# Kernel optimization log

Hardware: AMD Instinct MI355X
Metric: run time of the kernel (lower is better)

## Reference

```python
import jax, jax.numpy as jnp
import numpy as np

N = 65536      # nodes
E = 1048576    # edges (avg degree 16)
B = 64         # graphs in batch
H = 128        # hidden
L = 3          # message-passing layers
MAXZ = 100


def _segment_mean(x, idx, n):
    s = jax.ops.segment_sum(x, idx, num_segments=n)
    c = jax.ops.segment_sum(jnp.ones((idx.shape[0], 1), x.dtype), idx, num_segments=n)
    return s / jnp.maximum(c, 1.0)


def setup_inputs() -> dict:
    key = jax.random.key(0)
    ks = jax.random.split(key, 24)
    w = lambda k, shape: jax.random.normal(k, shape, dtype=jnp.float32) * 0.05
    inp = {
        "pos": jax.random.normal(ks[0], (N, 3), dtype=jnp.float32),
        "z": jax.random.randint(ks[1], (N,), 0, MAXZ),
        "batch": jnp.sort(jax.random.randint(ks[2], (N,), 0, B)),
        "edge_index": jax.random.randint(ks[3], (2, E), 0, N),
        "node_type": jax.random.randint(ks[4], (N,), 0, 2),
        # parameters (weights stored [in, out] so y = x @ W + b)
        "emb": w(ks[5], (MAXZ, H)),
        "lin_in_w": w(ks[6], (H + 3, H)),
        "lin_in_b": jnp.zeros((H,), jnp.float32),
        "msg_w1": w(ks[7], (L, 2 * H + 1, H)),
        "msg_b1": jnp.zeros((L, H), jnp.float32),
        "msg_w2": w(ks[8], (L, H, H)),
        "msg_b2": jnp.zeros((L, H), jnp.float32),
        "upd_w": w(ks[9], (L, 2 * H, H)),
        "upd_b": jnp.zeros((L, H), jnp.float32),
        "ro_w1": w(ks[10], (H, H)),
        "ro_b1": jnp.zeros((H,), jnp.float32),
        "ro_w2": w(ks[11], (H, 1)),
        "ro_b2": jnp.zeros((1,), jnp.float32),
    }
    return inp


def reference(pos, z, batch, edge_index, node_type,
              emb, lin_in_w, lin_in_b,
              msg_w1, msg_b1, msg_w2, msg_b2,
              upd_w, upd_b, ro_w1, ro_b1, ro_w2, ro_b2):
    # centroid-centered positions per graph
    center = _segment_mean(pos, batch, B)           # [B,3]
    pos_rel = pos - center[batch]                   # [N,3]

    x = jnp.concatenate([emb[z], pos_rel], axis=-1) @ lin_in_w + lin_in_b  # [N,H]

    row, col = edge_index[0], edge_index[1]
    rel = pos_rel[col] - pos_rel[row]               # [E,3]
    dist = jnp.linalg.norm(rel, axis=-1, keepdims=True)  # [E,1]

    for l in range(L):
        m_in = jnp.concatenate([x[col], x[row], dist], axis=-1)      # [E,2H+1]
        h = jax.nn.relu(m_in @ msg_w1[l] + msg_b1[l])
        m_ij = jax.nn.relu(h @ msg_w2[l] + msg_b2[l])                # [E,H] (dropout=identity, eval)
        m_i = _segment_mean(m_ij, row, N)                            # [N,H]
        x = jax.nn.relu(jnp.concatenate([x, m_i], axis=-1) @ upd_w[l] + upd_b[l])

    lig_mask = (node_type == 1).astype(x.dtype)                      # [N]
    lig_counts = jnp.maximum(jax.ops.segment_sum(lig_mask, batch, num_segments=B), 1.0)
    g = jax.ops.segment_sum(x * lig_mask[:, None], batch, num_segments=B)  # [B,H]
    g = g / lig_counts[:, None]

    hg = jax.nn.relu(g @ ro_w1 + ro_b1)
    affinity = (hg @ ro_w2 + ro_b2).squeeze(-1)                      # [B]
    return affinity
```

## Files before the change

kernel.cpp:

```cpp
#include <hip/hip_runtime.h>
#include <hip/hip_bf16.h>
#include <hip/hip_fp16.h>
#include <math.h>

#define NN 65536
#define NE 1048576
#define NB 64
#define HD 128
#define NL 3

#define O_CSUM   0
#define O_CCNT   192
#define O_LCNT   256
#define O_GSUM   320
#define O_DEGI   8512
#define O_POSREL 74048
#define O_RC     270656
#define O_XHI    1319232
#define O_XLO    5513536
#define O_P      9707840
#define O_RCD    13902144
#define O_Q      18096448
#define O_C1H    22290752
#define O_EW     22291456
#define O_MSUM   26485056
#define O_W2T    34873664
#define O_W1TH   34898240
#define O_W1TL   34947392
#define O_WUTH   34996544
#define O_WUTL   35045696
#define O_CHK    35094848

typedef __attribute__((ext_vector_type(8))) short bf16x8;
typedef __attribute__((ext_vector_type(8))) _Float16 f16x8;
typedef __attribute__((ext_vector_type(8))) unsigned short u16x8;
typedef __attribute__((ext_vector_type(4))) float f32x4;

__device__ __forceinline__ void atomAdd(float* p, float v) { unsafeAtomicAdd(p, v); }

__device__ __forceinline__ unsigned short f2bf(float f) {
    union { __hip_bfloat16 h; unsigned short u; } cv;
    cv.h = __float2bfloat16(f);
    return cv.u;
}
__device__ __forceinline__ float bf2f(unsigned short u) {
    union { float f; unsigned v; } c; c.v = ((unsigned)u) << 16; return c.f;
}
__device__ __forceinline__ void split2(float v, unsigned short& h, unsigned short& l) {
    h = f2bf(v); l = f2bf(v - bf2f(h));
}
__device__ __forceinline__ unsigned short f2h(float f) {
    union { __half h; unsigned short u; } c; c.h = __float2half(f); return c.u;
}

__global__ __launch_bounds__(256) void stats_kernel(
    const float* __restrict__ pos, const int* __restrict__ batch,
    const int* __restrict__ ntype,
    float* __restrict__ csum, float* __restrict__ ccnt, float* __restrict__ lcnt)
{
    __shared__ float s[NB * 5];
    const int tid = threadIdx.x;
    for (int i = tid; i < NB * 5; i += 256) s[i] = 0.f;
    __syncthreads();
    const int n = blockIdx.x * 256 + tid;
    const int b = batch[n];
    atomicAdd(&s[b*5+0], pos[n*3+0]);
    atomicAdd(&s[b*5+1], pos[n*3+1]);
    atomicAdd(&s[b*5+2], pos[n*3+2]);
    atomicAdd(&s[b*5+3], 1.f);
    if (ntype[n] == 1) atomicAdd(&s[b*5+4], 1.f);
    __syncthreads();
    for (int i = tid; i < NB * 5; i += 256) {
        float v = s[i];
        if (v != 0.f) {
            int b2 = i / 5, f = i - b2*5;
            if (f < 3)       atomAdd(&csum[b2*3+f], v);
            else if (f == 3) atomAdd(&ccnt[b2], v);
            else             atomAdd(&lcnt[b2], v);
        }
    }
}

__global__ __launch_bounds__(256) void deg_kernel(const int* __restrict__ row, int* __restrict__ degi)
{
    const int e = blockIdx.x * 256 + threadIdx.x;
    atomicAdd(&degi[row[e]], 1);
}

__global__ __launch_bounds__(256) void scanA_kernel(const int* __restrict__ degi, int* __restrict__ chunkSum)
{
    __shared__ int red[4];
    const int t = threadIdx.x, b = blockIdx.x;
    int v = degi[b*256 + t];
    #pragma unroll
    for (int off = 32; off > 0; off >>= 1) v += __shfl_down(v, off, 64);
    if ((t & 63) == 0) red[t >> 6] = v;
    __syncthreads();
    if (t == 0) chunkSum[b] = red[0] + red[1] + red[2] + red[3];
}

__global__ __launch_bounds__(256) void scanB_kernel(int* __restrict__ chunkSum)
{
    __shared__ int s[256];
    const int t = threadIdx.x;
    const int v = chunkSum[t];
    s[t] = v;
    __syncthreads();
    #pragma unroll
    for (int off = 1; off < 256; off <<= 1) {
        int u = (t >= off) ? s[t - off] : 0;
        __syncthreads();
        s[t] += u;
        __syncthreads();
    }
    chunkSum[t] = s[t] - v;
}

__global__ __launch_bounds__(256) void scanC_kernel(const int* __restrict__ degi,
                                                    const int* __restrict__ chunkOff,
                                                    int* __restrict__ rowStart)
{
    __shared__ int s[256];
    const int t = threadIdx.x, b = blockIdx.x;
    const int v = degi[b*256 + t];
    s[t] = v;
    __syncthreads();
    #pragma unroll
    for (int off = 1; off < 256; off <<= 1) {
        int u = (t >= off) ? s[t - off] : 0;
        __syncthreads();
        s[t] += u;
        __syncthreads();
    }
    rowStart[b*256 + t] = chunkOff[b] + s[t] - v;
}

__global__ __launch_bounds__(256) void scatter_kernel(
    const int* __restrict__ row, const int* __restrict__ col,
    const int* __restrict__ rowStart, int* __restrict__ cnt,
    uint2* __restrict__ rcD,
    const float* __restrict__ posrel)
{
    const int e = blockIdx.x * 256 + threadIdx.x;
    const int r = row[e], c = col[e];
    const float dx = posrel[c*3+0] - posrel[r*3+0];
    const float dy = posrel[c*3+1] - posrel[r*3+1];
    const float dz = posrel[c*3+2] - posrel[r*3+2];
    const float dist = sqrtf(dx*dx + dy*dy + dz*dz);
    const int p = rowStart[r] + atomicAdd(&cnt[r], 1);
    rcD[p] = make_uint2(((unsigned)r << 16) | (unsigned)c, __float_as_uint(dist));
}

__global__ __launch_bounds__(256) void posrel_kernel(
    const float* __restrict__ pos, const int* __restrict__ batch,
    const float* __restrict__ csum, const float* __restrict__ ccnt,
    float* __restrict__ posrel)
{
    const int n = blockIdx.x * 256 + threadIdx.x;
    const int b = batch[n];
    const float inv = 1.f / fmaxf(ccnt[b], 1.f);
    posrel[n*3+0] = pos[n*3+0] - csum[b*3+0]*inv;
    posrel[n*3+1] = pos[n*3+1] - csum[b*3+1]*inv;
    posrel[n*3+2] = pos[n*3+2] - csum[b*3+2]*inv;
}

__global__ __launch_bounds__(256) void wprep_kernel(
    const float* __restrict__ mw1, const float* __restrict__ uw,
    const float* __restrict__ mw2,
    const float* __restrict__ lin_w, const float* __restrict__ lin_b,
    const float* __restrict__ emb,
    unsigned short* __restrict__ w1th, unsigned short* __restrict__ w1tl,
    unsigned short* __restrict__ wuth, unsigned short* __restrict__ wutl,
    unsigned short* __restrict__ w2t, unsigned short* __restrict__ c1h,
    float* __restrict__ EW)
{
    const int idx = blockIdx.x * 256 + threadIdx.x;
    {
        const int l = idx >> 15, rem = idx & 32767;
        const int w = rem & 7, t = rem >> 3;
        const int c = t & 255, kb = t >> 8;
        const int k = kb*8 + w;
        const int kk = (c < 128) ? k : (128 + k);
        const int cc = c & 127;
        const float v = mw1[l*257*128 + kk*128 + cc];
        unsigned short h, lo; split2(v, h, lo);
        w1th[idx] = h; w1tl[idx] = lo;
    }
    {
        const int l = idx >> 15, rem = idx & 32767;
        const int w = rem & 7, t = rem >> 3;
        const int c = t & 127, kb = t >> 7;
        const int k = kb*8 + w;
        const float v = uw[l*256*128 + k*128 + c];
        unsigned short h, lo; split2(v, h, lo);
        wuth[idx] = h; wutl[idx] = lo;
    }
    if (idx < 49152) {
        const int l = idx >> 14, rem = idx & 16383;
        const int blk = rem >> 3, win = rem & 7;
        const int n = blk >> 4, cs = blk & 15;
        const int c = cs ^ (n & 7);
        const int k = c*8 + win;
        w2t[idx] = f2h(mw2[(l << 14) + k*128 + n]);
    }
    if (idx < 384) {
        const int l = idx >> 7, c = idx & 127;
        c1h[idx] = f2h(mw1[l*257*128 + 256*128 + c]);
    }
    if (idx < 12800) {
        const int j = idx & 127, zz = idx >> 7;
        float acc = lin_b[j];
        for (int k = 0; k < 128; ++k)
            acc += emb[zz*128 + k] * lin_w[k*128 + j];
        EW[idx] = acc;
    }
}

__global__ __launch_bounds__(256) void lin_in_kernel(
    const float* __restrict__ EW, const float* __restrict__ posrel,
    const int* __restrict__ zidx, const float* __restrict__ lin_w,
    unsigned short* __restrict__ xhi, unsigned short* __restrict__ xlo)
{
    const int tid = threadIdx.x;
    const int node = blockIdx.x * 16 + (tid >> 4);
    const int j0 = (tid & 15) * 8;

    const int zz = zidx[node];
    const float px = posrel[node*3+0], py = posrel[node*3+1], pz = posrel[node*3+2];

    const float4 e0 = *(const float4*)&EW[zz*128 + j0];
    const float4 e1 = *(const float4*)&EW[zz*128 + j0 + 4];
    const float4 wx0 = *(const float4*)&lin_w[128*128 + j0];
    const float4 wx1 = *(const float4*)&lin_w[128*128 + j0 + 4];
    const float4 wy0 = *(const float4*)&lin_w[129*128 + j0];
    const float4 wy1 = *(const float4*)&lin_w[129*128 + j0 + 4];
    const float4 wz0 = *(const float4*)&lin_w[130*128 + j0];
    const float4 wz1 = *(const float4*)&lin_w[130*128 + j0 + 4];

    float o[8];
    o[0] = e0.x + px*wx0.x + py*wy0.x + pz*wz0.x;
    o[1] = e0.y + px*wx0.y + py*wy0.y + pz*wz0.y;
    o[2] = e0.z + px*wx0.z + py*wy0.z + pz*wz0.z;
    o[3] = e0.w + px*wx0.w + py*wy0.w + pz*wz0.w;
    o[4] = e1.x + px*wx1.x + py*wy1.x + pz*wz1.x;
    o[5] = e1.y + px*wx1.y + py*wy1.y + pz*wz1.y;
    o[6] = e1.z + px*wx1.z + py*wy1.z + pz*wz1.z;
    o[7] = e1.w + px*wx1.w + py*wy1.w + pz*wz1.w;

    ushort4 h0, l0, h1, l1;
    split2(o[0], h0.x, l0.x); split2(o[1], h0.y, l0.y);
    split2(o[2], h0.z, l0.z); split2(o[3], h0.w, l0.w);
    split2(o[4], h1.x, l1.x); split2(o[5], h1.y, l1.y);
    split2(o[6], h1.z, l1.z); split2(o[7], h1.w, l1.w);
    *(ushort4*)&xhi[node*HD + j0]     = h0;
    *(ushort4*)&xhi[node*HD + j0 + 4] = h1;
    *(ushort4*)&xlo[node*HD + j0]     = l0;
    *(ushort4*)&xlo[node*HD + j0 + 4] = l1;
}

__global__ __launch_bounds__(256) void pq_gemm(
    const unsigned short* __restrict__ xhi, const unsigned short* __restrict__ xlo,
    const unsigned short* __restrict__ w1th, const unsigned short* __restrict__ w1tl,
    unsigned short* __restrict__ Ph, unsigned short* __restrict__ Qh,
    float* __restrict__ msum, const float* __restrict__ b1)
{
    const int tid = threadIdx.x;
    const int l = tid & 63, w = tid >> 6;
    const int mr = l & 15, qd = l >> 4;
    const int n0 = blockIdx.x * 64;
    const int c0 = w * 64;

    {
        float4* mz = (float4*)&msum[(long)blockIdx.x * 8192];
        const float4 z4 = make_float4(0.f, 0.f, 0.f, 0.f);
        #pragma unroll
        for (int it = 0; it < 8; ++it) mz[tid + it*256] = z4;
    }

    f32x4 acc[4][4];
    #pragma unroll
    for (int mt = 0; mt < 4; ++mt)
        #pragma unroll
        for (int nt = 0; nt < 4; ++nt) acc[mt][nt] = (f32x4){0.f,0.f,0.f,0.f};

    #pragma unroll
    for (int ks = 0; ks < 4; ++ks) {
        const int kof = ks*32 + qd*8;
        const int kb  = ks*4 + qd;
        bf16x8 ah[4], al[4], bh[4], bl[4];
        #pragma unroll
        for (int mt = 0; mt < 4; ++mt) {
            const int node = n0 + mt*16 + mr;
            ah[mt] = *(const bf16x8*)&xhi[node*HD + kof];
            al[mt] = *(const bf16x8*)&xlo[node*HD + kof];
        }
        #pragma unroll
        for (int nt = 0; nt < 4; ++nt) {
            const int c = c0 + nt*16 + mr;
            bh[nt] = *(const bf16x8*)&w1th[(kb << 11) + (c << 3)];
            bl[nt] = *(const bf16x8*)&w1tl[(kb << 11) + (c << 3)];
        }
        #pragma unroll
        for (int mt = 0; mt < 4; ++mt)
            #pragma unroll
            for (int nt = 0; nt < 4; ++nt) {
                acc[mt][nt] = __builtin_amdgcn_mfma_f32_16x16x32_bf16(bh[nt], ah[mt], acc[mt][nt], 0,0,0);
                acc[mt][nt] = __builtin_amdgcn_mfma_f32_16x16x32_bf16(bl[nt], ah[mt], acc[mt][nt], 0,0,0);
                acc[mt][nt] = __builtin_amdgcn_mfma_f32_16x16x32_bf16(bh[nt], al[mt], acc[mt][nt], 0,0,0);
            }
    }

    unsigned short* __restrict__ dst = (w < 2) ? Ph : Qh;
    const int cbase = (w < 2) ? c0 : c0 - 128;
    #pragma unroll
    for (int mt = 0; mt < 4; ++mt) {
        const int node = n0 + mt*16 + mr;
        #pragma unroll
        for (int nt = 0; nt < 4; ++nt) {
            const int ccb = cbase + nt*16 + qd*4;
            float4 bb4 = make_float4(0.f, 0.f, 0.f, 0.f);
            if (w >= 2) bb4 = *(const float4*)&b1[ccb];
            ushort4 o4;
            o4.x = f2h(acc[mt][nt][0] + bb4.x);
            o4.y = f2h(acc[mt][nt][1] + bb4.y);
            o4.z = f2h(acc[mt][nt][2] + bb4.z);
            o4.w = f2h(acc[mt][nt][3] + bb4.w);
            *(ushort4*)&dst[(long)node*HD + ccb] = o4;
        }
    }
}

__global__ __launch_bounds__(256) void upd_gemm(
    unsigned short* __restrict__ xhi, unsigned short* __restrict__ xlo,
    const float* __restrict__ msum, const int* __restrict__ degi,
    const unsigned short* __restrict__ wuth, const unsigned short* __restrict__ wutl,
    const float* __restrict__ bias)
{
    const int tid = threadIdx.x;
    const int l = tid & 63, w = tid >> 6;
    const int mr = l & 15, qd = l >> 4;
    const int n0 = blockIdx.x * 64 + w*16;
    const int node = n0 + mr;
    const float inv = 1.f / fmaxf((float)degi[node], 1.f);

    f32x4 acc[8];
    #pragma unroll
    for (int nt = 0; nt < 8; ++nt) acc[nt] = (f32x4){0.f,0.f,0.f,0.f};

    #pragma unroll 1
    for (int ks = 0; ks < 8; ++ks) {
        const int kof = ks*32 + qd*8;
        const int kb  = ks*4 + qd;
        bf16x8 ah, al;
        if (ks < 4) {
            ah = *(const bf16x8*)&xhi[node*HD + kof];
            al = *(const bf16x8*)&xlo[node*HD + kof];
        } else {
            const int mk = kof - 128;
            const float4 v0 = *(const float4*)&msum[(long)node*HD + mk];
            const float4 v1 = *(const float4*)&msum[(long)node*HD + mk + 4];
            union { bf16x8 v; unsigned short u[8]; } hh, ll;
            float vv[8] = { v0.x*inv, v0.y*inv, v0.z*inv, v0.w*inv,
                            v1.x*inv, v1.y*inv, v1.z*inv, v1.w*inv };
            #pragma unroll
            for (int i = 0; i < 8; ++i) split2(vv[i], hh.u[i], ll.u[i]);
            ah = hh.v; al = ll.v;
        }
        #pragma unroll
        for (int nt = 0; nt < 8; ++nt) {
            const int c = nt*16 + mr;
            const bf16x8 bh = *(const bf16x8*)&wuth[(kb << 10) + (c << 3)];
            const bf16x8 bl = *(const bf16x8*)&wutl[(kb << 10) + (c << 3)];
            acc[nt] = __builtin_amdgcn_mfma_f32_16x16x32_bf16(bh, ah, acc[nt], 0,0,0);
            acc[nt] = __builtin_amdgcn_mfma_f32_16x16x32_bf16(bl, ah, acc[nt], 0,0,0);
            acc[nt] = __builtin_amdgcn_mfma_f32_16x16x32_bf16(bh, al, acc[nt], 0,0,0);
        }
    }

    #pragma unroll
    for (int nt = 0; nt < 8; ++nt) {
        const int cb = nt*16 + qd*4;
        const float4 bb4 = *(const float4*)&bias[cb];
        float o0 = fmaxf(acc[nt][0] + bb4.x, 0.f);
        float o1 = fmaxf(acc[nt][1] + bb4.y, 0.f);
        float o2 = fmaxf(acc[nt][2] + bb4.z, 0.f);
        float o3 = fmaxf(acc[nt][3] + bb4.w, 0.f);
        ushort4 h4, l4;
        split2(o0, h4.x, l4.x); split2(o1, h4.y, l4.y);
        split2(o2, h4.z, l4.z); split2(o3, h4.w, l4.w);
        *(ushort4*)&xhi[(long)node*HD + cb] = h4;
        *(ushort4*)&xlo[(long)node*HD + cb] = l4;
    }
}

__global__ __launch_bounds__(256, 2) void edge_msg_kernel(
    const unsigned short* __restrict__ Ph, const unsigned short* __restrict__ Qh,
    const uint2* __restrict__ rcD,
    const unsigned short* __restrict__ c1h,
    const unsigned short* __restrict__ w2t,
    const float* __restrict__ b2,
    float* __restrict__ msum)
{
    __shared__ __align__(16) unsigned short w2s[16384];
    const int tid = threadIdx.x;

    {
        const uint4* __restrict__ src = (const uint4*)w2t;
        uint4* dst = (uint4*)w2s;
        #pragma unroll
        for (int i = 0; i < 8; ++i) dst[tid + i*256] = src[tid + i*256];
    }

    const long e0 = (long)blockIdx.x * 256;
    const int l  = tid & 63;
    const int w  = tid >> 6;
    const int mr = l & 15;
    const int qd = l >> 4;
    const long ebase = e0 + w*64;

    const int aoff = ((mr >> 2) << 4) + (mr & 3);
    int ecol[4], erow[4];
    float edist[4];
    #pragma unroll
    for (int m = 0; m < 4; ++m) {
        const uint2 rd = rcD[ebase + aoff + m*4];
        erow[m] = (int)(rd.x >> 16); ecol[m] = (int)(rd.x & 0xffffu);
        edist[m] = __uint_as_float(rd.y);
    }

    u16x8 praw[4][4];
    #pragma unroll
    for (int m = 0; m < 4; ++m)
        #pragma unroll
        for (int kk = 0; kk < 4; ++kk)
            praw[m][kk] = *(const u16x8*)&Ph[(long)ecol[m]*HD + kk*32 + qd*8];

    unsigned rcv[16];
    {
        const uint4* rc4 = (const uint4*)&rcD[ebase + qd*16];
        #pragma unroll
        for (int i = 0; i < 8; ++i) {
            const uint4 v = rc4[i];
            rcv[i*2+0] = (v.x >> 16) << 7;
            rcv[i*2+1] = (v.z >> 16) << 7;
        }
    }
    unsigned sameMask = 0;
    #pragma unroll
    for (int i = 1; i < 16; ++i) if (rcv[i] == rcv[i-1]) sameMask |= (1u << i);

    float b2v[8];
    #pragma unroll
    for (int t = 0; t < 8; ++t) b2v[t] = b2[t*16 + mr];

    f16x8 c8[4];
    #pragma unroll
    for (int kk = 0; kk < 4; ++kk) {
        union { u16x8 raw; f16x8 v; } cu;
        cu.raw = ((const u16x8*)c1h)[kk*4 + qd];
        c8[kk] = cu.v;
    }

    const f16x8 z8 = {};
    f16x8 afr[4][4];
    #pragma unroll
    for (int m = 0; m < 4; ++m) {
        union { u16x8 raw; f16x8 v; } qu[4];
        #pragma unroll
        for (int kk = 0; kk < 4; ++kk)
            qu[kk].raw = *(const u16x8*)&Qh[(long)erow[m]*HD + kk*32 + qd*8];
        const _Float16 d16 = (_Float16)edist[m];
        #pragma unroll
        for (int kk = 0; kk < 4; ++kk) {
            union { u16x8 raw; f16x8 v; } pu; pu.raw = praw[m][kk];
            f16x8 s = pu.v + qu[kk].v + d16 * c8[kk];
            afr[m][kk] = __builtin_elementwise_max(s, z8);
        }
    }

    __syncthreads();

    #pragma unroll 1
    for (int t = 0; t < 8; ++t) {
        f16x8 bfr[4];
        #pragma unroll
        for (int kk = 0; kk < 4; ++kk) {
            const int c = kk*4 + qd;
            const int blk = (t*16 + mr)*16 + (c ^ (mr & 7));
            union { u16x8 raw; f16x8 v; } bu;
            bu.raw = *(const u16x8*)&w2s[blk*8];
            bfr[kk] = bu.v;
        }
        const int colg = t*16 + mr;
        const float bb = b2v[t];

        f32x4 acc[4];
        #pragma unroll
        for (int m = 0; m < 4; ++m) acc[m] = (f32x4){0.f, 0.f, 0.f, 0.f};
        #pragma unroll
        for (int kk = 0; kk < 4; ++kk)
            #pragma unroll
            for (int m = 0; m < 4; ++m)
                acc[m] = __builtin_amdgcn_mfma_f32_16x16x32_f16(afr[m][kk], bfr[kk], acc[m], 0, 0, 0);

        float run = 0.f;
        #pragma unroll
        for (int i = 0; i < 16; ++i) {
            const float v = fmaxf(acc[i>>2][i&3] + bb, 0.f);
            run = (sameMask & (1u << i)) ? run + v : v;
            if (!(sameMask & (2u << i)))
                atomAdd(&msum[(long)(rcv[i] + colg)], run);
        }
    }
}

__global__ __launch_bounds__(256) void gsum_kernel(
    const unsigned short* __restrict__ xhi, const unsigned short* __restrict__ xlo,
    const int* __restrict__ batch,
    const int* __restrict__ ntype, float* __restrict__ gsum)
{
    const int tid = threadIdx.x;
    const int cg = tid & 31;
    const int ns = tid >> 5;
    const int n0 = blockIdx.x * 512 + ns * 64;

    int bprev = -1;
    float4 run = make_float4(0.f, 0.f, 0.f, 0.f);
    for (int i = 0; i < 64; ++i) {
        const int n = n0 + i;
        if (ntype[n] != 1) continue;
        const int b = batch[n];
        const ushort4 h  = *(const ushort4*)&xhi[(long)n*HD + cg*4];
        const ushort4 lo = *(const ushort4*)&xlo[(long)n*HD + cg*4];
        float4 v;
        v.x = bf2f(h.x) + bf2f(lo.x);
        v.y = bf2f(h.y) + bf2f(lo.y);
        v.z = bf2f(h.z) + bf2f(lo.z);
        v.w = bf2f(h.w) + bf2f(lo.w);
        if (b != bprev) {
            if (bprev >= 0) {
                float* dst = &gsum[bprev*HD + cg*4];
                atomAdd(dst+0, run.x); atomAdd(dst+1, run.y);
                atomAdd(dst+2, run.z); atomAdd(dst+3, run.w);
            }
            bprev = b; run = v;
        } else {
            run.x += v.x; run.y += v.y; run.z += v.z; run.w += v.w;
        }
    }
    if (bprev >= 0) {
        float* dst = &gsum[bprev*HD + cg*4];
        atomAdd(dst+0, run.x); atomAdd(dst+1, run.y);
        atomAdd(dst+2, run.z); atomAdd(dst+3, run.w);
    }
}

__global__ __launch_bounds__(128) void readout_kernel(
    const float* __restrict__ gsum, const float* __restrict__ lcnt,
    const float* __restrict__ w1, const float* __restrict__ b1,
    const float* __restrict__ w2, const float* __restrict__ b2,
    float* __restrict__ out)
{
    __shared__ float gs[HD];
    __shared__ float red[2];
    const int b = blockIdx.x, j = threadIdx.x;
    gs[j] = gsum[b*HD + j] / fmaxf(lcnt[b], 1.f);
    __syncthreads();
    float acc = b1[j];
    for (int k = 0; k < HD; ++k) acc += gs[k]*w1[k*HD + j];
    float hg = fmaxf(acc, 0.f) * w2[j];
    #pragma unroll
    for (int off = 32; off > 0; off >>= 1) hg += __shfl_down(hg, off, 64);
    if ((j & 63) == 0) red[j >> 6] = hg;
    __syncthreads();
    if (j == 0) out[b] = red[0] + red[1] + b2[0];
}

extern "C" void kernel_launch(void* const* d_in, const int* in_sizes, int n_in,
                              void* d_out, int out_size, void* d_ws, size_t ws_size,
                              hipStream_t stream)
{
    const float* pos   = (const float*)d_in[0];
    const int*   z     = (const int*)d_in[1];
    const int*   batch = (const int*)d_in[2];
    const int*   eidx  = (const int*)d_in[3];
    const int*   ntype = (const int*)d_in[4];
    const float* emb   = (const float*)d_in[5];
    const float* lin_w = (const float*)d_in[6];
    const float* lin_b = (const float*)d_in[7];
    const float* mw1   = (const float*)d_in[8];
    const float* mb1   = (const float*)d_in[9];
    const float* mw2   = (const float*)d_in[10];
    const float* mb2   = (const float*)d_in[11];
    const float* uw    = (const float*)d_in[12];
    const float* ub    = (const float*)d_in[13];
    const float* rw1   = (const float*)d_in[14];
    const float* rb1   = (const float*)d_in[15];
    const float* rw2   = (const float*)d_in[16];
    const float* rb2   = (const float*)d_in[17];

    const int* row = eidx;
    const int* col = eidx + NE;

    float* ws     = (float*)d_ws;
    float* csum   = ws + O_CSUM;
    float* ccnt   = ws + O_CCNT;
    float* lcnt   = ws + O_LCNT;
    float* gsum   = ws + O_GSUM;
    int*   degi   = (int*)(ws + O_DEGI);
    float* posrel = ws + O_POSREL;
    unsigned short* xhi = (unsigned short*)(ws + O_XHI);
    unsigned short* xlo = (unsigned short*)(ws + O_XLO);
    unsigned short* Ph  = (unsigned short*)(ws + O_P);
    uint2* rcD    = (uint2*)(ws + O_RCD);
    unsigned short* Qh  = (unsigned short*)(ws + O_Q);
    unsigned short* c1h = (unsigned short*)(ws + O_C1H);
    float* EW     = ws + O_EW;
    float* msum   = ws + O_MSUM;
    unsigned short* w2t  = (unsigned short*)(ws + O_W2T);
    unsigned short* w1th = (unsigned short*)(ws + O_W1TH);
    unsigned short* w1tl = (unsigned short*)(ws + O_W1TL);
    unsigned short* wuth = (unsigned short*)(ws + O_WUTH);
    unsigned short* wutl = (unsigned short*)(ws + O_WUTL);
    int* chunkSum = (int*)(ws + O_CHK);
    int* rowStart = (int*)xhi;
    int* cnt      = (int*)xhi + NN;

    (void)hipMemsetAsync(ws, 0, (size_t)(O_DEGI + NN) * sizeof(float), stream);
    (void)hipMemsetAsync(cnt, 0, (size_t)NN * sizeof(int), stream);

    stats_kernel  <<<NN/256, 256, 0, stream>>>(pos, batch, ntype, csum, ccnt, lcnt);
    deg_kernel    <<<NE/256, 256, 0, stream>>>(row, degi);
    posrel_kernel <<<NN/256, 256, 0, stream>>>(pos, batch, csum, ccnt, posrel);
    scanA_kernel  <<<256, 256, 0, stream>>>(degi, chunkSum);
    scanB_kernel  <<<1, 256, 0, stream>>>(chunkSum);
    scanC_kernel  <<<256, 256, 0, stream>>>(degi, chunkSum, rowStart);
    scatter_kernel<<<NE/256, 256, 0, stream>>>(row, col, rowStart, cnt, rcD, posrel);
    wprep_kernel  <<<384, 256, 0, stream>>>(mw1, uw, mw2, lin_w, lin_b, emb,
                                            w1th, w1tl, wuth, wutl, w2t, c1h, EW);

    lin_in_kernel<<<NN/16, 256, 0, stream>>>(EW, posrel, z, lin_w, xhi, xlo);

    for (int l = 0; l < NL; ++l) {
        pq_gemm<<<NN/64, 256, 0, stream>>>(xhi, xlo,
                                           w1th + (size_t)l*32768, w1tl + (size_t)l*32768,
                                           Ph, Qh, msum, mb1 + (size_t)l*HD);
        edge_msg_kernel<<<NE/256, 256, 0, stream>>>(Ph, Qh, rcD,
                                                    c1h + (size_t)l*HD,
                                                    w2t + (size_t)l*16384, mb2 + l*HD, msum);
        upd_gemm<<<NN/64, 256, 0, stream>>>(xhi, xlo, msum, degi,
                                            wuth + (size_t)l*32768, wutl + (size_t)l*32768,
                                            ub + l*HD);
    }

    gsum_kernel   <<<NN/512, 256, 0, stream>>>(xhi, xlo, batch, ntype, gsum);
    readout_kernel<<<NB, 128, 0, stream>>>(gsum, lcnt, rw1, rb1, rw2, rb2, (float*)d_out);
}
```

Before: 701.5 us.

## Process two edge tiles per block and prefetch second tile's gathers during first

Each edge_msg block now handles 512 edges as two 256-edge tiles. It loads the second tile's indices and P rows before running the first tile's MFMA and atomic loop, then finishes the second tile. The aim is to hide gather latency behind compute and to amortize the per-block load of W2 into shared memory over twice as many edges. The extra live registers for the prefetched tile may push the kernel past the 2-blocks-per-SM launch bound and cause spills, and the grid is halved.

```diff
diff --git a/kernel.cpp b/kernel.cpp
--- a/kernel.cpp
+++ b/kernel.cpp
@@ -393,6 +393,54 @@
     }
 }
 
+#define EDGE_PHASE1(AFR, PRAW, EROW, EDIST)                                          \
+    _Pragma("unroll")                                                                \
+    for (int m = 0; m < 4; ++m) {                                                    \
+        union { u16x8 raw; f16x8 v; } qu[4];                                         \
+        _Pragma("unroll")                                                            \
+        for (int kk = 0; kk < 4; ++kk)                                               \
+            qu[kk].raw = *(const u16x8*)&Qh[(long)EROW[m]*HD + kk*32 + qd*8];        \
+        const _Float16 d16 = (_Float16)EDIST[m];                                     \
+        _Pragma("unroll")                                                            \
+        for (int kk = 0; kk < 4; ++kk) {                                             \
+            union { u16x8 raw; f16x8 v; } pu; pu.raw = PRAW[m][kk];                  \
+            f16x8 s = pu.v + qu[kk].v + d16 * c8[kk];                                \
+            AFR[m][kk] = __builtin_elementwise_max(s, z8);                           \
+        }                                                                            \
+    }
+
+#define EDGE_TLOOP(AFR, RCV, SAMEMASK)                                               \
+    _Pragma("unroll 1")                                                              \
+    for (int t = 0; t < 8; ++t) {                                                    \
+        f16x8 bfr[4];                                                                \
+        _Pragma("unroll")                                                            \
+        for (int kk = 0; kk < 4; ++kk) {                                             \
+            const int c = kk*4 + qd;                                                 \
+            const int blk = (t*16 + mr)*16 + (c ^ (mr & 7));                         \
+            union { u16x8 raw; f16x8 v; } bu;                                        \
+            bu.raw = *(const u16x8*)&w2s[blk*8];                                     \
+            bfr[kk] = bu.v;                                                          \
+        }                                                                            \
+        const int colg = t*16 + mr;                                                  \
+        const float bb = b2v[t];                                                     \
+        f32x4 acc[4];                                                                \
+        _Pragma("unroll")                                                            \
+        for (int m = 0; m < 4; ++m) acc[m] = (f32x4){0.f, 0.f, 0.f, 0.f};            \
+        _Pragma("unroll")                                                            \
+        for (int kk = 0; kk < 4; ++kk)                                               \
+            _Pragma("unroll")                                                        \
+            for (int m = 0; m < 4; ++m)                                              \
+                acc[m] = __builtin_amdgcn_mfma_f32_16x16x32_f16(AFR[m][kk], bfr[kk], acc[m], 0, 0, 0); \
+        float run = 0.f;                                                             \
+        _Pragma("unroll")                                                            \
+        for (int i = 0; i < 16; ++i) {                                               \
+            const float v = fmaxf(acc[i>>2][i&3] + bb, 0.f);                         \
+            run = (SAMEMASK & (1u << i)) ? run + v : v;                              \
+            if (!(SAMEMASK & (2u << i)))                                             \
+                atomAdd(&msum[(long)(RCV[i] + colg)], run);                          \
+        }                                                                            \
+    }
+
 __global__ __launch_bounds__(256, 2) void edge_msg_kernel(
     const unsigned short* __restrict__ Ph, const unsigned short* __restrict__ Qh,
     const uint2* __restrict__ rcD,
@@ -411,48 +459,48 @@
         for (int i = 0; i < 8; ++i) dst[tid + i*256] = src[tid + i*256];
     }
 
-    const long e0 = (long)blockIdx.x * 256;
+    const long e0 = (long)blockIdx.x * 512;
     const int l  = tid & 63;
     const int w  = tid >> 6;
     const int mr = l & 15;
     const int qd = l >> 4;
-    const long ebase = e0 + w*64;
+    const long ebaseA = e0 + w*64;
+    const long ebaseB = e0 + 256 + w*64;
 
     const int aoff = ((mr >> 2) << 4) + (mr & 3);
-    int ecol[4], erow[4];
-    float edist[4];
+
+    int ecolA[4], erowA[4];
+    float edistA[4];
     #pragma unroll
     for (int m = 0; m < 4; ++m) {
-        const uint2 rd = rcD[ebase + aoff + m*4];
-        erow[m] = (int)(rd.x >> 16); ecol[m] = (int)(rd.x & 0xffffu);
-        edist[m] = __uint_as_float(rd.y);
-    }
-
-    u16x8 praw[4][4];
+        const uint2 rd = rcD[ebaseA + aoff + m*4];
+        erowA[m] = (int)(rd.x >> 16); ecolA[m] = (int)(rd.x & 0xffffu);
+        edistA[m] = __uint_as_float(rd.y);
+    }
+    u16x8 prawA[4][4];
     #pragma unroll
     for (int m = 0; m < 4; ++m)
         #pragma unroll
         for (int kk = 0; kk < 4; ++kk)
-            praw[m][kk] = *(const u16x8*)&Ph[(long)ecol[m]*HD + kk*32 + qd*8];
-
-    unsigned rcv[16];
+            prawA[m][kk] = *(const u16x8*)&Ph[(long)ecolA[m]*HD + kk*32 + qd*8];
+
+    unsigned rcvA[16];
     {
-        const uint4* rc4 = (const uint4*)&rcD[ebase + qd*16];
+        const uint4* rc4 = (const uint4*)&rcD[ebaseA + qd*16];
         #pragma unroll
         for (int i = 0; i < 8; ++i) {
             const uint4 v = rc4[i];
-            rcv[i*2+0] = (v.x >> 16) << 7;
-            rcv[i*2+1] = (v.z >> 16) << 7;
-        }
-    }
-    unsigned sameMask = 0;
-    #pragma unroll
-    for (int i = 1; i < 16; ++i) if (rcv[i] == rcv[i-1]) sameMask |= (1u << i);
+            rcvA[i*2+0] = (v.x >> 16) << 7;
+            rcvA[i*2+1] = (v.z >> 16) << 7;
+        }
+    }
+    unsigned sameMaskA = 0;
+    #pragma unroll
+    for (int i = 1; i < 16; ++i) if (rcvA[i] == rcvA[i-1]) sameMaskA |= (1u << i);
 
     float b2v[8];
     #pragma unroll
     for (int t = 0; t < 8; ++t) b2v[t] = b2[t*16 + mr];
-
     f16x8 c8[4];
     #pragma unroll
     for (int kk = 0; kk < 4; ++kk) {
@@ -462,56 +510,47 @@
     }
 
     const f16x8 z8 = {};
-    f16x8 afr[4][4];
+
+    f16x8 afrA[4][4];
+    EDGE_PHASE1(afrA, prawA, erowA, edistA)
+
+    int ecolB[4], erowB[4];
+    float edistB[4];
     #pragma unroll
     for (int m = 0; m < 4; ++m) {
-        union { u16x8 raw; f16x8 v; } qu[4];
+        const uint2 rd = rcD[ebaseB + aoff + m*4];
+        erowB[m] = (int)(rd.x >> 16); ecolB[m] = (int)(rd.x & 0xffffu);
+        edistB[m] = __uint_as_float(rd.y);
+    }
+    u16x8 prawB[4][4];
+    #pragma unroll
+    for (int m = 0; m < 4; ++m)
         #pragma unroll
         for (int kk = 0; kk < 4; ++kk)
-            qu[kk].raw = *(const u16x8*)&Qh[(long)erow[m]*HD + kk*32 + qd*8];
-        const _Float16 d16 = (_Float16)edist[m];
-        #pragma unroll
-        for (int kk = 0; kk < 4; ++kk) {
-            union { u16x8 raw; f16x8 v; } pu; pu.raw = praw[m][kk];
-            f16x8 s = pu.v + qu[kk].v + d16 * c8[kk];
-            afr[m][kk] = __builtin_elementwise_max(s, z8);
-        }
-    }
-
-    __syncthreads();
-
-    #pragma unroll 1
-    for (int t = 0; t < 8; ++t) {
-        f16x8 bfr[4];
-        #pragma unroll
-        for (int kk = 0; kk < 4; ++kk) {
-            const int c = kk*4 + qd;
-            const int blk = (t*16 + mr)*16 + (c ^ (mr & 7));
-            union { u16x8 raw; f16x8 v; } bu;
-            bu.raw = *(const u16x8*)&w2s[blk*8];
-            bfr[kk] = bu.v;
-        }
-        const int colg = t*16 + mr;
-        const float bb = b2v[t];
-
-        f32x4 acc[4];
-        #pragma unroll
-        for (int m = 0; m < 4; ++m) acc[m] = (f32x4){0.f, 0.f, 0.f, 0.f};
-        #pragma unroll
-        for (int kk = 0; kk < 4; ++kk)
-            #pragma unroll
-            for (int m = 0; m < 4; ++m)
-                acc[m] = __builtin_amdgcn_mfma_f32_16x16x32_f16(afr[m][kk], bfr[kk], acc[m], 0, 0, 0);
-
-        float run = 0.f;
-        #pragma unroll
-        for (int i = 0; i < 16; ++i) {
-            const float v = fmaxf(acc[i>>2][i&3] + bb, 0.f);
-            run = (sameMask & (1u << i)) ? run + v : v;
-            if (!(sameMask & (2u << i)))
-                atomAdd(&msum[(long)(rcv[i] + colg)], run);
-        }
-    }
+            prawB[m][kk] = *(const u16x8*)&Ph[(long)ecolB[m]*HD + kk*32 + qd*8];
+
+    unsigned rcvB[16];
+    {
+        const uint4* rc4 = (const uint4*)&rcD[ebaseB + qd*16];
+        #pragma unroll
+        for (int i = 0; i < 8; ++i) {
+            const uint4 v = rc4[i];
+            rcvB[i*2+0] = (v.x >> 16) << 7;
+            rcvB[i*2+1] = (v.z >> 16) << 7;
+        }
+    }
+    unsigned sameMaskB = 0;
+    #pragma unroll
+    for (int i = 1; i < 16; ++i) if (rcvB[i] == rcvB[i-1]) sameMaskB |= (1u << i);
+
+    __syncthreads();
+
+    EDGE_TLOOP(afrA, rcvA, sameMaskA)
+
+    f16x8 afrB[4][4];
+    EDGE_PHASE1(afrB, prawB, erowB, edistB)
+
+    EDGE_TLOOP(afrB, rcvB, sameMaskB)
 }
 
 __global__ __launch_bounds__(256) void gsum_kernel(
@@ -645,7 +684,7 @@
         pq_gemm<<<NN/64, 256, 0, stream>>>(xhi, xlo,
                                            w1th + (size_t)l*32768, w1tl + (size_t)l*32768,
                                            Ph, Qh, msum, mb1 + (size_t)l*HD);
-        edge_msg_kernel<<<NE/256, 256, 0, stream>>>(Ph, Qh, rcD,
+        edge_msg_kernel<<<NE/512, 256, 0, stream>>>(Ph, Qh, rcD,
                                                     c1h + (size_t)l*HD,
                                                     w2t + (size_t)l*16384, mb2 + l*HD, msum);
         upd_gemm<<<NN/64, 256, 0, stream>>>(xhi, xlo, msum, degi,
```

After: 776.6 us. 10.7% more time.
